# Kernel optimization log

Measured on AMD Instinct MI355X. Metric: run time of the kernel, lower is better.

## Reference

```python
import jax, jax.numpy as jnp
import numpy as np

B, S, D, H = 2, 2048, 2048, 16
DK = D // H
THETA = 10000.0


def setup_inputs() -> dict:
    key = jax.random.key(0)
    ks = jax.random.split(key, 5)
    scale = 0.02
    return {
        "x": jax.random.normal(ks[0], (B, S, D), dtype=jnp.float32),
        "W_Q": jax.random.normal(ks[1], (D, D), dtype=jnp.float32) * scale,
        "W_K": jax.random.normal(ks[2], (D, D), dtype=jnp.float32) * scale,
        "W_V": jax.random.normal(ks[3], (D, D), dtype=jnp.float32) * scale,
        "W_O": jax.random.normal(ks[4], (D, D), dtype=jnp.float32) * scale,
        "token_positions": jnp.arange(S, dtype=jnp.int32),
    }


def _rope(x, pos):
    # x: [B, S, H, DK]; pos: [S]. Interleaved-pair rotation (cs336 RoPE).
    half = DK // 2
    inv_freq = THETA ** (-(jnp.arange(half, dtype=jnp.float32) / half))  # [half]
    ang = pos.astype(jnp.float32)[:, None] * inv_freq[None, :]           # [S, half]
    cos = jnp.cos(ang)[None, :, None, :]                                 # [1,S,1,half]
    sin = jnp.sin(ang)[None, :, None, :]
    x1, x2 = x[..., ::2], x[..., 1::2]
    r1 = x1 * cos - x2 * sin
    r2 = x1 * sin + x2 * cos
    return jnp.stack([r1, r2], axis=-1).reshape(x.shape)


def reference(x, W_Q, W_K, W_V, W_O, token_positions):
    # QKV projections (Linear with no bias: y = x @ W^T)
    Q = (x @ W_Q.T).reshape(B, S, H, DK)
    K = (x @ W_K.T).reshape(B, S, H, DK)
    V = (x @ W_V.T).reshape(B, S, H, DK)
    Q = _rope(Q, token_positions)
    K = _rope(K, token_positions)
    scores = jnp.einsum("bqhd,bkhd->bhqk", Q, K) / jnp.sqrt(jnp.float32(DK))
    causal = jnp.tril(jnp.ones((S, S), dtype=bool))  # True = attend
    scores = jnp.where(causal[None, None], scores, -jnp.inf)
    attn = jax.nn.softmax(scores, axis=-1)
    out = jnp.einsum("bhqk,bkhd->bqhd", attn, V).reshape(B, S, D)
    return out @ W_O.T
```

## Files before the change

### kernel.cpp

```cpp
#include <hip/hip_runtime.h>
#include <hip/hip_bf16.h>
#include <cstdint>
#include <cstddef>

#define B_ 2
#define S_ 2048
#define D_ 2048
#define H_ 16
#define DK_ 128
#define M_ (B_*S_)

typedef __attribute__((ext_vector_type(8))) __bf16 bf16x8;
typedef __attribute__((ext_vector_type(4))) float f32x4;
typedef __attribute__((ext_vector_type(16))) float f32x16;

__device__ __forceinline__ unsigned short f2bf(float f) {
  union { float f; unsigned int u; } v; v.f = f;
  unsigned int r = (v.u + 0x7fffu + ((v.u >> 16) & 1u)) >> 16;
  return (unsigned short)r;
}
__device__ __forceinline__ float bf2f(unsigned short b) {
  union { unsigned int u; float f; } v; v.u = ((unsigned int)b) << 16;
  return v.f;
}

__device__ __forceinline__ void gld16(const void* g, void* l) {
  __builtin_amdgcn_global_load_lds(
      (const __attribute__((address_space(1))) unsigned int*)g,
      (__attribute__((address_space(3))) unsigned int*)l, 16, 0, 0);
}

__global__ void cvt_bf16(const float* __restrict__ src, unsigned short* __restrict__ dst, int n) {
  int i = (blockIdx.x * blockDim.x + threadIdx.x) * 4;
  if (i + 3 < n) {
    float4 v = *(const float4*)(src + i);
    dst[i+0] = f2bf(v.x); dst[i+1] = f2bf(v.y);
    dst[i+2] = f2bf(v.z); dst[i+3] = f2bf(v.w);
  }
}

template<int WRITE_BF16>
__global__ __launch_bounds__(256) void gemm_bt(const unsigned short* __restrict__ A,
                                               const unsigned short* __restrict__ W0,
                                               const unsigned short* __restrict__ W1,
                                               const unsigned short* __restrict__ W2,
                                               void* __restrict__ C0, void* __restrict__ C1,
                                               void* __restrict__ C2,
                                               int M, int N, int K) {
  __shared__ unsigned short sA[128 * 32];
  __shared__ unsigned short sB[128 * 32];
  const int z = blockIdx.z;
  const unsigned short* Bt = (z == 0) ? W0 : (z == 1) ? W1 : W2;
  void* Cout = (z == 0) ? C0 : (z == 1) ? C1 : C2;

  const int tid  = threadIdx.x;
  const int lane = tid & 63;
  const int wid  = tid >> 6;
  const int wm = wid >> 1, wn = wid & 1;
  const int quad = lane >> 4, l16 = lane & 15;
  const int bm = blockIdx.y * 128, bn = blockIdx.x * 128;
  const int srow = lane >> 2;
  const int scol = (lane & 3) * 8;

  f32x4 acc[4][4];
  #pragma unroll
  for (int i = 0; i < 4; ++i)
    #pragma unroll
    for (int j = 0; j < 4; ++j)
      acc[i][j] = (f32x4){0.f, 0.f, 0.f, 0.f};

  for (int k0 = 0; k0 < K; k0 += 32) {
    __syncthreads();
    #pragma unroll
    for (int p = 0; p < 2; ++p) {
      int row = p * 64 + wid * 16;
      gld16(A  + (size_t)(bm + row + srow) * K + k0 + scol, sA + row * 32);
      gld16(Bt + (size_t)(bn + row + srow) * K + k0 + scol, sB + row * 32);
    }
    __syncthreads();

    bf16x8 af[4], bfr[4];
    #pragma unroll
    for (int i = 0; i < 4; ++i)
      af[i] = *(const bf16x8*)(sA + (wm * 64 + i * 16 + l16) * 32 + quad * 8);
    #pragma unroll
    for (int j = 0; j < 4; ++j)
      bfr[j] = *(const bf16x8*)(sB + (wn * 64 + j * 16 + l16) * 32 + quad * 8);
    #pragma unroll
    for (int i = 0; i < 4; ++i)
      #pragma unroll
      for (int j = 0; j < 4; ++j)
        acc[i][j] = __builtin_amdgcn_mfma_f32_16x16x32_bf16(af[i], bfr[j], acc[i][j], 0, 0, 0);
  }

  #pragma unroll
  for (int i = 0; i < 4; ++i) {
    int row = bm + wm * 64 + i * 16 + quad * 4;
    #pragma unroll
    for (int j = 0; j < 4; ++j) {
      int col = bn + wn * 64 + j * 16 + l16;
      #pragma unroll
      for (int r = 0; r < 4; ++r) {
        if (WRITE_BF16)
          ((unsigned short*)Cout)[(size_t)(row + r) * N + col] = f2bf(acc[i][j][r]);
        else
          ((float*)Cout)[(size_t)(row + r) * N + col] = acc[i][j][r];
      }
    }
  }
}

__global__ void rope_kernel(unsigned short* __restrict__ Q, unsigned short* __restrict__ K,
                            const int* __restrict__ pos) {
  int idx = blockIdx.x * blockDim.x + threadIdx.x;
  int i = idx & 63;
  int h = (idx >> 6) & (H_ - 1);
  int s = (idx >> 10) & (S_ - 1);
  int b = idx >> 21;
  float p = (float)pos[s];
  float inv = expf(-(float)i * (9.210340371976184f / 64.0f));
  float ang = p * inv;
  float sn, cs;
  sincosf(ang, &sn, &cs);
  size_t base = (((size_t)b * S_ + s) * D_) + (size_t)h * DK_ + 2 * i;
  float x1 = bf2f(Q[base]), x2 = bf2f(Q[base + 1]);
  Q[base]     = f2bf(x1 * cs - x2 * sn);
  Q[base + 1] = f2bf(x1 * sn + x2 * cs);
  x1 = bf2f(K[base]); x2 = bf2f(K[base + 1]);
  K[base]     = f2bf(x1 * cs - x2 * sn);
  K[base + 1] = f2bf(x1 * sn + x2 * cs);
}

__global__ __launch_bounds__(256) void transpose_bf16(const unsigned short* __restrict__ src,
                                                      unsigned short* __restrict__ dst) {
  __shared__ unsigned short sT[64 * 64];
  const int b = blockIdx.y;
  const int tx = blockIdx.x & 31, ty = blockIdx.x >> 5;
  const size_t base = (size_t)b * 2048 * 2048;
  const int m0 = ty * 64, c0 = tx * 64;
  const int tid = threadIdx.x;
  #pragma unroll
  for (int c = 0; c < 2; ++c) {
    int idx = tid + c * 256;
    int row = idx >> 3;
    int chk = idx & 7;
    uint4 v = *(const uint4*)(src + base + (size_t)(m0 + row) * 2048 + c0 + chk * 8);
    *(uint4*)(sT + row * 64 + ((chk ^ (row & 7)) * 8)) = v;
  }
  __syncthreads();
  #pragma unroll
  for (int c = 0; c < 2; ++c) {
    int idx = tid + c * 256;
    int orow = idx >> 3;
    int ocol = (idx & 7) * 8;
    unsigned short tmp[8];
    #pragma unroll
    for (int j = 0; j < 8; ++j) {
      int lr = ocol + j;
      int lc = orow;
      tmp[j] = sT[lr * 64 + (((lc >> 3) ^ (lr & 7)) * 8) + (lc & 7)];
    }
    *(uint4*)(dst + base + (size_t)(c0 + orow) * 2048 + m0 + ocol) = *(const uint4*)tmp;
  }
}

__global__ __launch_bounds__(256, 2) void flash_attn(const unsigned short* __restrict__ Q,
                                                     const unsigned short* __restrict__ K,
                                                     const unsigned short* __restrict__ VT,
                                                     unsigned short* __restrict__ O) {
  __shared__ unsigned short sK[2][64 * 128];
  __shared__ unsigned short sVT[2][128 * 64];
  __shared__ unsigned short sP[4][32 * 64];

  const int tid = threadIdx.x, lane = tid & 63, wid = tid >> 6;
  const int half = lane >> 5, l32 = lane & 31;
  const int qi = 15 - (blockIdx.x & 15);
  const int bh = blockIdx.x >> 4;
  const int h = bh & (H_ - 1), b = bh >> 4;
  const int qw = qi * 128 + wid * 32;
  const size_t qkbase = ((size_t)b * S_) * D_ + (size_t)h * DK_;
  const unsigned short* Qg = Q + qkbase;
  const unsigned short* Kg = K + qkbase;
  const unsigned short* VTg = VT + (size_t)bh * DK_ * S_;
  unsigned short* Og = O + qkbase;
  unsigned short* sPw = sP[wid];

  const int kKeySub = lane >> 4;
  const int kPhys   = lane & 15;
  const int vFeatSub = lane >> 3;
  const int vPhys    = lane & 7;

  bf16x8 qf[8];
  #pragma unroll
  for (int ks = 0; ks < 8; ++ks)
    qf[ks] = *(const bf16x8*)(Qg + (size_t)(qw + l32) * D_ + ks * 16 + half * 8);

  union { unsigned short u[8]; bf16x8 v; } onesu;
  #pragma unroll
  for (int j = 0; j < 8; ++j) onesu.u[j] = 0x3F80;
  const bf16x8 ones = onesu.v;

  f32x16 Oacc[4];
  #pragma unroll
  for (int ft = 0; ft < 4; ++ft)
    #pragma unroll
    for (int r = 0; r < 16; ++r) Oacc[ft][r] = 0.f;
  f32x16 l_acc;
  #pragma unroll
  for (int r = 0; r < 16; ++r) l_acc[r] = 0.f;
  const float scale = 0.08838834764831845f;

  const int nkb = 2 * (qi + 1);

  auto stage = [&](int kb) {
    const int k0 = kb * 64;
    unsigned short* bK = sK[kb & 1];
    unsigned short* bV = sVT[kb & 1];
    #pragma unroll
    for (int p = 0; p < 4; ++p) {
      int issue = wid * 4 + p;
      int key = issue * 4 + kKeySub;
      int logiK = (kPhys & 8) | ((kPhys ^ key) & 7);
      gld16(Kg + (size_t)(k0 + key) * D_ + logiK * 8, bK + issue * 512);
      int feat = issue * 8 + vFeatSub;
      int logiV = vPhys ^ (feat & 7);
      gld16(VTg + (size_t)feat * S_ + k0 + logiV * 8, bV + issue * 512);
    }
  };

  stage(0);

  for (int kb = 0; kb < nkb; ++kb) {
    __syncthreads();
    if (kb + 1 < nkb) stage(kb + 1);

    const int k0 = kb * 64;
    if (k0 > qw + 31) continue;

    const unsigned short* bK = sK[kb & 1];
    const unsigned short* bV = sVT[kb & 1];

    f32x16 sc[2];
    #pragma unroll
    for (int t = 0; t < 2; ++t)
      #pragma unroll
      for (int r = 0; r < 16; ++r) sc[t][r] = 0.f;
    #pragma unroll
    for (int ks = 0; ks < 8; ++ks) {
      const int logi = ks * 2 + half;
      #pragma unroll
      for (int t = 0; t < 2; ++t) {
        const int key = t * 32 + l32;
        const int phys = (logi & 8) | ((logi ^ key) & 7);
        bf16x8 kf = *(const bf16x8*)(bK + key * 128 + phys * 8);
        sc[t] = __builtin_amdgcn_mfma_f32_32x32x16_bf16(qf[ks], kf, sc[t], 0, 0, 0);
      }
    }

    const bool diag = (k0 + 63 > qw);
    #pragma unroll
    for (int t = 0; t < 2; ++t) {
      const int col = t * 32 + l32;
      const int keyg = k0 + col;
      #pragma unroll
      for (int r = 0; r < 16; ++r) {
        const int rl = (r & 3) + 8 * (r >> 2) + 4 * half;
        float v = sc[t][r] * scale;
        if (diag && (keyg > qw + rl)) v = -1e30f;
        sPw[rl * 64 + (((col >> 3) ^ (rl & 7)) * 8) + (col & 7)] = f2bf(__expf(v));
      }
    }

    #pragma unroll
    for (int ksp = 0; ksp < 4; ++ksp) {
      const int logi = ksp * 2 + half;
      bf16x8 pf = *(const bf16x8*)(sPw + l32 * 64 + ((logi ^ (l32 & 7)) * 8));
      l_acc = __builtin_amdgcn_mfma_f32_32x32x16_bf16(pf, ones, l_acc, 0, 0, 0);
      #pragma unroll
      for (int ft = 0; ft < 4; ++ft) {
        const int feat = ft * 32 + l32;
        const int phys = logi ^ (feat & 7);
        bf16x8 vf = *(const bf16x8*)(bV + feat * 64 + phys * 8);
        Oacc[ft] = __builtin_amdgcn_mfma_f32_32x32x16_bf16(pf, vf, Oacc[ft], 0, 0, 0);
      }
    }
  }

  #pragma unroll
  for (int ft = 0; ft < 4; ++ft) {
    const int feat = ft * 32 + l32;
    #pragma unroll
    for (int r = 0; r < 16; ++r) {
      const int rl = (r & 3) + 8 * (r >> 2) + 4 * half;
      Og[(size_t)(qw + rl) * D_ + feat] = f2bf(Oacc[ft][r] / l_acc[r]);
    }
  }
}

extern "C" void kernel_launch(void* const* d_in, const int* in_sizes, int n_in,
                              void* d_out, int out_size, void* d_ws, size_t ws_size,
                              hipStream_t stream) {
  const float* x  = (const float*)d_in[0];
  const float* Wq = (const float*)d_in[1];
  const float* Wk = (const float*)d_in[2];
  const float* Wv = (const float*)d_in[3];
  const float* Wo = (const float*)d_in[4];
  const int*  pos = (const int*)d_in[5];
  float* out = (float*)d_out;

  char* ws = (char*)d_ws;
  size_t off = 0;
  auto alloc = [&](size_t bytes) { void* p = ws + off; off += (bytes + 255) & ~255ULL; return p; };
  const size_t nx = (size_t)M_ * D_;
  const size_t nw = (size_t)D_ * D_;
  unsigned short* xb  = (unsigned short*)alloc(nx * 2);
  unsigned short* wqb = (unsigned short*)alloc(nw * 2);
  unsigned short* wkb = (unsigned short*)alloc(nw * 2);
  unsigned short* wvb = (unsigned short*)alloc(nw * 2);
  unsigned short* wob = (unsigned short*)alloc(nw * 2);
  unsigned short* Qb  = (unsigned short*)alloc(nx * 2);
  unsigned short* Kb  = (unsigned short*)alloc(nx * 2);
  unsigned short* Vb  = (unsigned short*)alloc(nx * 2);
  unsigned short* AOb = xb;
  unsigned short* VTb = wqb;

  hipLaunchKernelGGL(cvt_bf16, dim3(nx / 1024), dim3(256), 0, stream, x,  xb,  (int)nx);
  hipLaunchKernelGGL(cvt_bf16, dim3(nw / 1024), dim3(256), 0, stream, Wq, wqb, (int)nw);
  hipLaunchKernelGGL(cvt_bf16, dim3(nw / 1024), dim3(256), 0, stream, Wk, wkb, (int)nw);
  hipLaunchKernelGGL(cvt_bf16, dim3(nw / 1024), dim3(256), 0, stream, Wv, wvb, (int)nw);
  hipLaunchKernelGGL(cvt_bf16, dim3(nw / 1024), dim3(256), 0, stream, Wo, wob, (int)nw);

  hipLaunchKernelGGL((gemm_bt<1>), dim3(D_ / 128, M_ / 128, 3), dim3(256), 0, stream,
                     xb, wqb, wkb, wvb, (void*)Qb, (void*)Kb, (void*)Vb, M_, D_, D_);

  hipLaunchKernelGGL(rope_kernel, dim3((B_ * S_ * H_ * 64) / 256), dim3(256), 0, stream, Qb, Kb, pos);

  hipLaunchKernelGGL(transpose_bf16, dim3(1024, 2), dim3(256), 0, stream, Vb, VTb);

  hipLaunchKernelGGL(flash_attn, dim3(B_ * H_ * (S_ / 128)), dim3(256), 0, stream, Qb, Kb, VTb, AOb);

  hipLaunchKernelGGL((gemm_bt<0>), dim3(D_ / 128, M_ / 128, 1), dim3(256), 0, stream,
                     AOb, wob, wob, wob, (void*)out, (void*)out, (void*)out, M_, D_, D_);
}
```

Baseline: 459.6 us.

## Rewrite projection GEMM as 256x256 tile, 8-wave, double-buffered pipelined kernel

Replaces the simple 128x128 single-buffered GEMM with a 256x256 tile, 512-thread kernel using double-buffered LDS with async global-to-LDS prefetch interleaved across four compute phases. It adds an XOR swizzle of the LDS layout to avoid bank conflicts, and s_setprio around the MFMA bursts. The aim is to hide global load latency and raise data reuse per tile for the QKV and output projections. The costs are higher register and LDS pressure, 64 KB of LDS and 128 accumulator floats per thread. There is also a risk from hand-tuned waitcnt and barrier correctness.

```diff
diff --git a/kernel.cpp b/kernel.cpp
--- a/kernel.cpp
+++ b/kernel.cpp
@@ -40,15 +40,15 @@
 }
 
 template<int WRITE_BF16>
-__global__ __launch_bounds__(256) void gemm_bt(const unsigned short* __restrict__ A,
-                                               const unsigned short* __restrict__ W0,
-                                               const unsigned short* __restrict__ W1,
-                                               const unsigned short* __restrict__ W2,
-                                               void* __restrict__ C0, void* __restrict__ C1,
-                                               void* __restrict__ C2,
-                                               int M, int N, int K) {
-  __shared__ unsigned short sA[128 * 32];
-  __shared__ unsigned short sB[128 * 32];
+__global__ __launch_bounds__(512, 2) void gemm8p(const unsigned short* __restrict__ A,
+                                                 const unsigned short* __restrict__ W0,
+                                                 const unsigned short* __restrict__ W1,
+                                                 const unsigned short* __restrict__ W2,
+                                                 void* __restrict__ C0, void* __restrict__ C1,
+                                                 void* __restrict__ C2,
+                                                 int M, int N, int K) {
+  __shared__ unsigned short sA[2][2][256 * 32];
+  __shared__ unsigned short sB[2][2][256 * 32];
   const int z = blockIdx.z;
   const unsigned short* Bt = (z == 0) ? W0 : (z == 1) ? W1 : W2;
   void* Cout = (z == 0) ? C0 : (z == 1) ? C1 : C2;
@@ -56,55 +56,95 @@
   const int tid  = threadIdx.x;
   const int lane = tid & 63;
   const int wid  = tid >> 6;
-  const int wm = wid >> 1, wn = wid & 1;
-  const int quad = lane >> 4, l16 = lane & 15;
-  const int bm = blockIdx.y * 128, bn = blockIdx.x * 128;
+  const int wm = wid >> 2, wn = wid & 3;
+  const int l16 = lane & 15, quad = lane >> 4;
+  const int col16 = quad ^ ((lane >> 1) & 3);
+  const int qk_log = (lane & 3) ^ ((lane >> 3) & 3);
   const int srow = lane >> 2;
-  const int scol = (lane & 3) * 8;
-
-  f32x4 acc[4][4];
-  #pragma unroll
-  for (int i = 0; i < 4; ++i)
+  const int bm = blockIdx.y * 256, bn = blockIdx.x * 256;
+  const int NT = K >> 6;
+
+  f32x4 acc[8][4];
+  #pragma unroll
+  for (int i = 0; i < 8; ++i)
     #pragma unroll
     for (int j = 0; j < 4; ++j)
       acc[i][j] = (f32x4){0.f, 0.f, 0.f, 0.f};
 
-  for (int k0 = 0; k0 < K; k0 += 32) {
-    __syncthreads();
+  auto stage = [&](const unsigned short* __restrict__ g, int rowbase,
+                   unsigned short* l, int t, int kh) {
+    const unsigned short* src = g + (size_t)rowbase * K + t * 64 + kh * 32 + qk_log * 8;
     #pragma unroll
     for (int p = 0; p < 2; ++p) {
-      int row = p * 64 + wid * 16;
-      gld16(A  + (size_t)(bm + row + srow) * K + k0 + scol, sA + row * 32);
-      gld16(Bt + (size_t)(bn + row + srow) * K + k0 + scol, sB + row * 32);
-    }
-    __syncthreads();
-
-    bf16x8 af[4], bfr[4];
-    #pragma unroll
-    for (int i = 0; i < 4; ++i)
-      af[i] = *(const bf16x8*)(sA + (wm * 64 + i * 16 + l16) * 32 + quad * 8);
-    #pragma unroll
-    for (int j = 0; j < 4; ++j)
-      bfr[j] = *(const bf16x8*)(sB + (wn * 64 + j * 16 + l16) * 32 + quad * 8);
-    #pragma unroll
-    for (int i = 0; i < 4; ++i)
-      #pragma unroll
-      for (int j = 0; j < 4; ++j)
-        acc[i][j] = __builtin_amdgcn_mfma_f32_16x16x32_bf16(af[i], bfr[j], acc[i][j], 0, 0, 0);
-  }
-
-  #pragma unroll
-  for (int i = 0; i < 4; ++i) {
-    int row = bm + wm * 64 + i * 16 + quad * 4;
-    #pragma unroll
-    for (int j = 0; j < 4; ++j) {
-      int col = bn + wn * 64 + j * 16 + l16;
+      const int i = wid * 2 + p;
+      gld16(src + (size_t)(i * 16 + srow) * K, l + i * 512);
+    }
+  };
+
+  stage(A,  bm, &sA[0][0][0], 0, 0);
+  stage(Bt, bn, &sB[0][0][0], 0, 0);
+  stage(A,  bm, &sA[0][1][0], 0, 1);
+  stage(Bt, bn, &sB[0][1][0], 0, 1);
+  stage(A,  bm, &sA[1][0][0], 1, 0);
+  stage(Bt, bn, &sB[1][0][0], 1, 0);
+  asm volatile("s_waitcnt vmcnt(4)" ::: "memory");
+  __builtin_amdgcn_s_barrier();
+
+  for (int t = 0; t < NT; ++t) {
+    const int buf = t & 1;
+    bf16x8 bfrag[4];
+    #pragma unroll
+    for (int ph = 0; ph < 4; ++ph) {
+      const int ks = ph >> 1;
+      const int mh = ph & 1;
+      bf16x8 afrag[4];
+      const unsigned short* aP = &sA[buf][ks][0] +
+          (size_t)((wm * 128 + mh * 64 + l16) * 4 + col16) * 8;
+      #pragma unroll
+      for (int mf = 0; mf < 4; ++mf)
+        afrag[mf] = *(const bf16x8*)(aP + mf * 512);
+      if (mh == 0) {
+        const unsigned short* bP = &sB[buf][ks][0] +
+            (size_t)((wn * 64 + l16) * 4 + col16) * 8;
+        #pragma unroll
+        for (int nf = 0; nf < 4; ++nf)
+          bfrag[nf] = *(const bf16x8*)(bP + nf * 512);
+      }
+      if (ph == 0)      { if (t + 1 < NT) stage(A,  bm, &sA[buf ^ 1][1][0], t + 1, 1); }
+      else if (ph == 1) { if (t + 1 < NT) stage(Bt, bn, &sB[buf ^ 1][1][0], t + 1, 1); }
+      else if (ph == 2) { if (t + 2 < NT) stage(A,  bm, &sA[buf][0][0],     t + 2, 0); }
+      else              { if (t + 2 < NT) stage(Bt, bn, &sB[buf][0][0],     t + 2, 0); }
+
+      __builtin_amdgcn_s_barrier();
+      asm volatile("s_waitcnt lgkmcnt(0)" ::: "memory");
+      __builtin_amdgcn_s_setprio(1);
+      #pragma unroll
+      for (int nf = 0; nf < 4; ++nf)
+        #pragma unroll
+        for (int mf = 0; mf < 4; ++mf)
+          acc[mh * 4 + mf][nf] = __builtin_amdgcn_mfma_f32_16x16x32_bf16(
+              afrag[mf], bfrag[nf], acc[mh * 4 + mf][nf], 0, 0, 0);
+      __builtin_amdgcn_s_setprio(0);
+      if (ph == 3) {
+        if (t + 2 < NT) asm volatile("s_waitcnt vmcnt(4)" ::: "memory");
+        else            asm volatile("s_waitcnt vmcnt(0)" ::: "memory");
+      }
+      __builtin_amdgcn_s_barrier();
+    }
+  }
+
+  #pragma unroll
+  for (int mf = 0; mf < 8; ++mf) {
+    const int row = bm + wm * 128 + mf * 16 + quad * 4;
+    #pragma unroll
+    for (int nf = 0; nf < 4; ++nf) {
+      const int col = bn + wn * 64 + nf * 16 + l16;
       #pragma unroll
       for (int r = 0; r < 4; ++r) {
         if (WRITE_BF16)
-          ((unsigned short*)Cout)[(size_t)(row + r) * N + col] = f2bf(acc[i][j][r]);
+          ((unsigned short*)Cout)[(size_t)(row + r) * N + col] = f2bf(acc[mf][nf][r]);
         else
-          ((float*)Cout)[(size_t)(row + r) * N + col] = acc[i][j][r];
+          ((float*)Cout)[(size_t)(row + r) * N + col] = acc[mf][nf][r];
       }
     }
   }
@@ -330,7 +370,7 @@
   hipLaunchKernelGGL(cvt_bf16, dim3(nw / 1024), dim3(256), 0, stream, Wv, wvb, (int)nw);
   hipLaunchKernelGGL(cvt_bf16, dim3(nw / 1024), dim3(256), 0, stream, Wo, wob, (int)nw);
 
-  hipLaunchKernelGGL((gemm_bt<1>), dim3(D_ / 128, M_ / 128, 3), dim3(256), 0, stream,
+  hipLaunchKernelGGL((gemm8p<1>), dim3(D_ / 256, M_ / 256, 3), dim3(512), 0, stream,
                      xb, wqb, wkb, wvb, (void*)Qb, (void*)Kb, (void*)Vb, M_, D_, D_);
 
   hipLaunchKernelGGL(rope_kernel, dim3((B_ * S_ * H_ * 64) / 256), dim3(256), 0, stream, Qb, Kb, pos);
@@ -339,6 +379,6 @@
 
   hipLaunchKernelGGL(flash_attn, dim3(B_ * H_ * (S_ / 128)), dim3(256), 0, stream, Qb, Kb, VTb, AOb);
 
-  hipLaunchKernelGGL((gemm_bt<0>), dim3(D_ / 128, M_ / 128, 1), dim3(256), 0, stream,
+  hipLaunchKernelGGL((gemm8p<0>), dim3(D_ / 256, M_ / 256, 1), dim3(512), 0, stream,
                      AOb, wob, wob, wob, (void*)out, (void*)out, (void*)out, M_, D_, D_);
 }
```

New measurement: 455.8 us. No clear change (-0.8%).
